# Kernel optimization log

Hardware: AMD Instinct MI355X
Metric: run time of the kernel (lower is better)

The kernel has to match this reference:

```python
import jax, jax.numpy as jnp
import numpy as np

P_DIMS = [100, 100, 80, 60, 60]
P = sum(P_DIMS)  # 400
N_STREAMS = len(P_DIMS)
MEM_ITERS = 5
DECAY = 0.8
LR = 0.5        # hebbian_learning_rate
FORGET = 0.9999 # hebbian_forget_rate
NEG_SLOPE = 0.01


def _build_masks():
    idx = np.cumsum([0] + P_DIMS)
    hier = np.zeros((P, P), np.float32)
    for i in range(N_STREAMS):
        for j in range(i, N_STREAMS):
            hier[idx[i]:idx[i + 1], idx[j]:idx[j + 1]] = 1.0
    iters = [MEM_ITERS - f for f in range(N_STREAMS)]  # [5,4,3,2,1]
    rmasks = np.zeros((MEM_ITERS, P), np.float32)
    for it in range(MEM_ITERS):
        for s, r in enumerate(iters):
            if it < r:
                rmasks[it, idx[s]:idx[s + 1]] = 1.0
    return jnp.asarray(hier), jnp.asarray(rmasks)


def setup_inputs() -> dict:
    key = jax.random.key(0)
    k1, k2, k3, k4 = jax.random.split(key, 4)
    B = 512
    return {
        'M_prev': jax.random.normal(k1, (B, P, P), dtype=jnp.float32) * 0.1,
        'p_inferred': jax.random.normal(k2, (B, P), dtype=jnp.float32),
        'p_generated': jax.random.normal(k3, (B, P), dtype=jnp.float32),
        'query': jax.random.normal(k4, (B, P), dtype=jnp.float32),
    }


def reference(M_prev, p_inferred, p_generated, query):
    hier_mask, retrieval_masks = _build_masks()

    # Hebbian update: M = clamp(forget*M_prev + lr*(p-phat)(p+phat)^T, -1, 1) * hier_mask
    outer = (p_inferred - p_generated)[:, :, None] * (p_inferred + p_generated)[:, None, :]
    M = jnp.clip(FORGET * M_prev + LR * outer, -1.0, 1.0) * hier_mask

    # Hierarchical attractor retrieval
    h = jax.nn.leaky_relu(jnp.clip(query, -1.0, 1.0), NEG_SLOPE)

    def step(h, mask):
        mv = jnp.einsum('bpq,bq->bp', M, h)
        upd = jax.nn.leaky_relu(jnp.clip(DECAY * h + mv, -1.0, 1.0), NEG_SLOPE)
        return (1.0 - mask) * h + mask * upd, None

    h, _ = jax.lax.scan(step, h, retrieval_masks)
    return h
```

## Files before the change

### kernel.cpp

```cpp
#include <hip/hip_runtime.h>


#define PDIM 400
#define CROWS 96
#define FORGET 0.9999f
#define LRATE  0.5f
#define DECAY  0.8f
#define SLOPE  0.01f

__device__ __forceinline__ float leaky_clip(float x) {
    x = fminf(fmaxf(x, -1.0f), 1.0f);
    return x > 0.0f ? x : SLOPE * x;
}
__device__ __forceinline__ float clamp1(float x) {
    return fminf(fmaxf(x, -1.0f), 1.0f);
}

__device__ __forceinline__ int c4beg(int p) {
    return (p < 100) ? 0 : (p < 200) ? 25 : (p < 280) ? 50 : (p < 340) ? 70 : 85;
}

__device__ __forceinline__ float wave_sum(float x) {
    x += __int_as_float(__builtin_amdgcn_update_dpp(0, __float_as_int(x), 0xB1,  0xf, 0xf, true));
    x += __int_as_float(__builtin_amdgcn_update_dpp(0, __float_as_int(x), 0x4E,  0xf, 0xf, true));
    x += __int_as_float(__builtin_amdgcn_update_dpp(0, __float_as_int(x), 0x141, 0xf, 0xf, true));
    x += __int_as_float(__builtin_amdgcn_update_dpp(0, __float_as_int(x), 0x140, 0xf, 0xf, true));
    x += __int_as_float(__builtin_amdgcn_update_dpp(0, __float_as_int(x), 0x142, 0xf, 0xf, true));
    x += __int_as_float(__builtin_amdgcn_update_dpp(0, __float_as_int(x), 0x143, 0xf, 0xf, true));
    return __int_as_float(__builtin_amdgcn_readlane(__float_as_int(x), 63));
}

__device__ __forceinline__ void load_row(const float* __restrict__ Mb,
                                         int p, int R, int l,
                                         int& c4, float4& A, float4& B) {
    const float4 z4 = make_float4(0.f, 0.f, 0.f, 0.f);
    c4 = 0; A = z4; B = z4;
    if (p < R) {
        c4 = c4beg(p);
        const float* __restrict__ row = Mb + (size_t)p * PDIM;
        if (l >= c4)                A = *(const float4*)(row + 4 * l);
        if (l < 36 && 64 + l >= c4) B = *(const float4*)(row + 256 + 4 * l);
    }
}

__global__ __launch_bounds__(512, 2)
void hier_mem_kernel(const float* __restrict__ M_prev,
                     const float* __restrict__ p_inf,
                     const float* __restrict__ p_gen,
                     const float* __restrict__ query,
                     float* __restrict__ out)
{
    __shared__ float s_mc[CROWS][PDIM];
    __shared__ float s_h[2][PDIM];
    __shared__ float s_la[PDIM];

    const int b   = blockIdx.x;
    const int tid = threadIdx.x;
    const int l   = tid & 63;
    const int wid = tid >> 6;
    const float* __restrict__ Mb = M_prev + (size_t)b * PDIM * PDIM;

    if (tid < PDIM) {
        const float pi = p_inf[b * PDIM + tid];
        const float pg = p_gen[b * PDIM + tid];
        s_la[tid]   = LRATE * (pi - pg);
        s_h[0][tid] = leaky_clip(query[b * PDIM + tid]);
    }

    const float4 z4 = make_float4(0.f, 0.f, 0.f, 0.f);
    const float4* __restrict__ pi4 = (const float4*)(p_inf + (size_t)b * PDIM);
    const float4* __restrict__ pg4 = (const float4*)(p_gen + (size_t)b * PDIM);
    float4 vA, vB = z4;
    {
        const float4 x = pi4[l], y = pg4[l];
        vA = make_float4(x.x + y.x, x.y + y.y, x.z + y.z, x.w + y.w);
        if (l < 36) {
            const float4 u = pi4[64 + l], v = pg4[64 + l];
            vB = make_float4(u.x + v.x, u.y + v.y, u.z + v.z, u.w + v.w);
        }
    }
    __syncthreads();

    {
        const float* __restrict__ hcur = s_h[0];
        float* __restrict__ hnew = s_h[1];
        float4 hA = *(const float4*)(hcur + 4 * l);
        float4 hB = z4;
        if (l < 36) hB = *(const float4*)(hcur + 256 + 4 * l);

        int p = wid;
        int c0, c1; float4 A0, B0, A1, B1;
        load_row(Mb, p,     PDIM, l, c0, A0, B0);
        load_row(Mb, p + 8, PDIM, l, c1, A1, B1);

        while (p < PDIM) {
            int c2; float4 A2, B2;
            load_row(Mb, p + 16, PDIM, l, c2, A2, B2);

            const float la = s_la[p];
            float acc = 0.f;
            float4 mA = z4, mB = z4;
            if (l >= c0) {
                mA.x = clamp1(fmaf(FORGET, A0.x, la * vA.x));
                mA.y = clamp1(fmaf(FORGET, A0.y, la * vA.y));
                mA.z = clamp1(fmaf(FORGET, A0.z, la * vA.z));
                mA.w = clamp1(fmaf(FORGET, A0.w, la * vA.w));
                acc = fmaf(mA.x, hA.x, fmaf(mA.y, hA.y, fmaf(mA.z, hA.z, mA.w * hA.w)));
            }
            if (l < 36 && 64 + l >= c0) {
                mB.x = clamp1(fmaf(FORGET, B0.x, la * vB.x));
                mB.y = clamp1(fmaf(FORGET, B0.y, la * vB.y));
                mB.z = clamp1(fmaf(FORGET, B0.z, la * vB.z));
                mB.w = clamp1(fmaf(FORGET, B0.w, la * vB.w));
                acc = fmaf(mB.x, hB.x, fmaf(mB.y, hB.y, fmaf(mB.z, hB.z, fmaf(mB.w, hB.w, acc))));
            }
            if (p < CROWS) {
                *(float4*)&s_mc[p][4 * l] = mA;
                if (l < 36) *(float4*)&s_mc[p][256 + 4 * l] = mB;
            }

            const float tot = wave_sum(acc);
            if (l == 0) {
                hnew[p] = leaky_clip(fmaf(DECAY, hcur[p], tot));
            }

            p += 8; c0 = c1; A0 = A1; B0 = B1; c1 = c2; A1 = A2; B1 = B2;
        }
        __syncthreads();
    }

    int cur = 1;
    const int Rt[4] = {340, 280, 200, 100};
    #pragma unroll
    for (int t = 0; t < 4; ++t) {
        const int R = Rt[t];
        const float* __restrict__ hcur = s_h[cur];
        float* __restrict__ hnew = s_h[cur ^ 1];

        float4 hA = *(const float4*)(hcur + 4 * l);
        float4 hB = z4;
        if (l < 36) hB = *(const float4*)(hcur + 256 + 4 * l);

        int sp = CROWS + wid;
        int c0, c1; float4 A0, B0, A1, B1;
        load_row(Mb, sp,     R, l, c0, A0, B0);
        load_row(Mb, sp + 8, R, l, c1, A1, B1);

        {
            int p = wid;
            float4 KA = *(const float4*)&s_mc[p][4 * l];
            float4 KB = z4;
            if (l < 36) KB = *(const float4*)&s_mc[p][256 + 4 * l];
            while (p < CROWS) {
                const int pn = p + 8;
                float4 NA = z4, NB = z4;
                if (pn < CROWS) {
                    NA = *(const float4*)&s_mc[pn][4 * l];
                    if (l < 36) NB = *(const float4*)&s_mc[pn][256 + 4 * l];
                }
                float acc = fmaf(KA.x, hA.x, fmaf(KA.y, hA.y, fmaf(KA.z, hA.z, KA.w * hA.w)));
                acc = fmaf(KB.x, hB.x, fmaf(KB.y, hB.y, fmaf(KB.z, hB.z, fmaf(KB.w, hB.w, acc))));
                const float tot = wave_sum(acc);
                if (l == 0) {
                    hnew[p] = leaky_clip(fmaf(DECAY, hcur[p], tot));
                }
                p = pn; KA = NA; KB = NB;
            }
        }

        while (sp < R) {
            int c2; float4 A2, B2;
            load_row(Mb, sp + 16, R, l, c2, A2, B2);

            const float la = s_la[sp];
            float acc = 0.f;
            if (l >= c0) {
                float m0 = clamp1(fmaf(FORGET, A0.x, la * vA.x));
                float m1 = clamp1(fmaf(FORGET, A0.y, la * vA.y));
                float m2 = clamp1(fmaf(FORGET, A0.z, la * vA.z));
                float m3 = clamp1(fmaf(FORGET, A0.w, la * vA.w));
                acc = fmaf(m0, hA.x, fmaf(m1, hA.y, fmaf(m2, hA.z, m3 * hA.w)));
            }
            if (l < 36 && 64 + l >= c0) {
                float m0 = clamp1(fmaf(FORGET, B0.x, la * vB.x));
                float m1 = clamp1(fmaf(FORGET, B0.y, la * vB.y));
                float m2 = clamp1(fmaf(FORGET, B0.z, la * vB.z));
                float m3 = clamp1(fmaf(FORGET, B0.w, la * vB.w));
                acc = fmaf(m0, hB.x, fmaf(m1, hB.y, fmaf(m2, hB.z, fmaf(m3, hB.w, acc))));
            }

            const float tot = wave_sum(acc);
            if (l == 0) {
                hnew[sp] = leaky_clip(fmaf(DECAY, hcur[sp], tot));
            }

            sp += 8; c0 = c1; A0 = A1; B0 = B1; c1 = c2; A1 = A2; B1 = B2;
        }

        if (tid >= R && tid < PDIM) hnew[tid] = hcur[tid];
        __syncthreads();
        cur ^= 1;
    }

    if (tid < PDIM) {
        out[b * PDIM + tid] = s_h[cur][tid];
    }
}

extern "C" void kernel_launch(void* const* d_in, const int* in_sizes, int n_in,
                              void* d_out, int out_size, void* d_ws, size_t ws_size,
                              hipStream_t stream) {
    const float* M_prev = (const float*)d_in[0];
    const float* p_inf  = (const float*)d_in[1];
    const float* p_gen  = (const float*)d_in[2];
    const float* query  = (const float*)d_in[3];
    float* out = (float*)d_out;

    const int B = in_sizes[1] / PDIM;
    hipLaunchKernelGGL(hier_mem_kernel, dim3(B), dim3(512), 0, stream,
                       M_prev, p_inf, p_gen, query, out);
}
```

Baseline: 503.7 us.

## Use packed FP32 math, shrink LDS row cache, raise occupancy to four blocks

Replaces scalar FMA chains with v_pk_fma/v_pk_mul packed FP32 inline asm. The shared-memory cache of updated M rows drops from 96 to 46 rows, and launch bounds now request 4 blocks per CU. Register prefetch depth in the later retrieval passes falls from two rows to one. The aim is more resident waves to hide global memory latency on the M_prev re-reads. In exchange, more rows must be re-read from global memory in each later pass, and prefetch depth per wave is lower.

```diff
diff --git a/kernel.cpp b/kernel.cpp
--- a/kernel.cpp
+++ b/kernel.cpp
@@ -2,18 +2,34 @@
 
 
 #define PDIM 400
-#define CROWS 96
+#define CROWS 46
 #define FORGET 0.9999f
 #define LRATE  0.5f
 #define DECAY  0.8f
 #define SLOPE  0.01f
 
+typedef float f32x2 __attribute__((ext_vector_type(2)));
+union V4 { float4 f4; f32x2 h2[2]; };
+
 __device__ __forceinline__ float leaky_clip(float x) {
     x = fminf(fmaxf(x, -1.0f), 1.0f);
     return x > 0.0f ? x : SLOPE * x;
 }
 __device__ __forceinline__ float clamp1(float x) {
     return fminf(fmaxf(x, -1.0f), 1.0f);
+}
+__device__ __forceinline__ f32x2 pk_mul(f32x2 a, f32x2 b) {
+    f32x2 d;
+    asm("v_pk_mul_f32 %0, %1, %2" : "=v"(d) : "v"(a), "v"(b));
+    return d;
+}
+__device__ __forceinline__ f32x2 pk_fma(f32x2 a, f32x2 b, f32x2 c) {
+    f32x2 d;
+    asm("v_pk_fma_f32 %0, %1, %2, %3" : "=v"(d) : "v"(a), "v"(b), "v"(c));
+    return d;
+}
+__device__ __forceinline__ f32x2 clamp2(f32x2 x) {
+    x.x = clamp1(x.x); x.y = clamp1(x.y); return x;
 }
 
 __device__ __forceinline__ int c4beg(int p) {
@@ -32,18 +48,19 @@
 
 __device__ __forceinline__ void load_row(const float* __restrict__ Mb,
                                          int p, int R, int l,
-                                         int& c4, float4& A, float4& B) {
-    const float4 z4 = make_float4(0.f, 0.f, 0.f, 0.f);
-    c4 = 0; A = z4; B = z4;
+                                         int& c4, V4& A, V4& B) {
+    A.f4 = make_float4(0.f, 0.f, 0.f, 0.f);
+    B.f4 = A.f4;
+    c4 = 0;
     if (p < R) {
         c4 = c4beg(p);
         const float* __restrict__ row = Mb + (size_t)p * PDIM;
-        if (l >= c4)                A = *(const float4*)(row + 4 * l);
-        if (l < 36 && 64 + l >= c4) B = *(const float4*)(row + 256 + 4 * l);
-    }
-}
-
-__global__ __launch_bounds__(512, 2)
+        if (l >= c4)                A.f4 = *(const float4*)(row + 4 * l);
+        if (l < 36 && 64 + l >= c4) B.f4 = *(const float4*)(row + 256 + 4 * l);
+    }
+}
+
+__global__ __launch_bounds__(512, 4)
 void hier_mem_kernel(const float* __restrict__ M_prev,
                      const float* __restrict__ p_inf,
                      const float* __restrict__ p_gen,
@@ -70,56 +87,56 @@
     const float4 z4 = make_float4(0.f, 0.f, 0.f, 0.f);
     const float4* __restrict__ pi4 = (const float4*)(p_inf + (size_t)b * PDIM);
     const float4* __restrict__ pg4 = (const float4*)(p_gen + (size_t)b * PDIM);
-    float4 vA, vB = z4;
+    V4 vA, vB; vB.f4 = z4;
     {
         const float4 x = pi4[l], y = pg4[l];
-        vA = make_float4(x.x + y.x, x.y + y.y, x.z + y.z, x.w + y.w);
+        vA.f4 = make_float4(x.x + y.x, x.y + y.y, x.z + y.z, x.w + y.w);
         if (l < 36) {
             const float4 u = pi4[64 + l], v = pg4[64 + l];
-            vB = make_float4(u.x + v.x, u.y + v.y, u.z + v.z, u.w + v.w);
-        }
-    }
+            vB.f4 = make_float4(u.x + v.x, u.y + v.y, u.z + v.z, u.w + v.w);
+        }
+    }
+    const f32x2 F2 = {FORGET, FORGET};
     __syncthreads();
 
     {
         const float* __restrict__ hcur = s_h[0];
         float* __restrict__ hnew = s_h[1];
-        float4 hA = *(const float4*)(hcur + 4 * l);
-        float4 hB = z4;
-        if (l < 36) hB = *(const float4*)(hcur + 256 + 4 * l);
+        V4 hA, hB; hB.f4 = z4;
+        hA.f4 = *(const float4*)(hcur + 4 * l);
+        if (l < 36) hB.f4 = *(const float4*)(hcur + 256 + 4 * l);
 
         int p = wid;
-        int c0, c1; float4 A0, B0, A1, B1;
+        int c0, c1; V4 A0, B0, A1, B1;
         load_row(Mb, p,     PDIM, l, c0, A0, B0);
         load_row(Mb, p + 8, PDIM, l, c1, A1, B1);
 
         while (p < PDIM) {
-            int c2; float4 A2, B2;
+            int c2; V4 A2, B2;
             load_row(Mb, p + 16, PDIM, l, c2, A2, B2);
 
             const float la = s_la[p];
-            float acc = 0.f;
-            float4 mA = z4, mB = z4;
+            const f32x2 la2 = {la, la};
+            f32x2 acc2 = {0.f, 0.f};
+            V4 mA, mB; mA.f4 = z4; mB.f4 = z4;
             if (l >= c0) {
-                mA.x = clamp1(fmaf(FORGET, A0.x, la * vA.x));
-                mA.y = clamp1(fmaf(FORGET, A0.y, la * vA.y));
-                mA.z = clamp1(fmaf(FORGET, A0.z, la * vA.z));
-                mA.w = clamp1(fmaf(FORGET, A0.w, la * vA.w));
-                acc = fmaf(mA.x, hA.x, fmaf(mA.y, hA.y, fmaf(mA.z, hA.z, mA.w * hA.w)));
+                mA.h2[0] = clamp2(pk_fma(F2, A0.h2[0], pk_mul(la2, vA.h2[0])));
+                mA.h2[1] = clamp2(pk_fma(F2, A0.h2[1], pk_mul(la2, vA.h2[1])));
+                acc2 = pk_fma(mA.h2[0], hA.h2[0], acc2);
+                acc2 = pk_fma(mA.h2[1], hA.h2[1], acc2);
             }
             if (l < 36 && 64 + l >= c0) {
-                mB.x = clamp1(fmaf(FORGET, B0.x, la * vB.x));
-                mB.y = clamp1(fmaf(FORGET, B0.y, la * vB.y));
-                mB.z = clamp1(fmaf(FORGET, B0.z, la * vB.z));
-                mB.w = clamp1(fmaf(FORGET, B0.w, la * vB.w));
-                acc = fmaf(mB.x, hB.x, fmaf(mB.y, hB.y, fmaf(mB.z, hB.z, fmaf(mB.w, hB.w, acc))));
+                mB.h2[0] = clamp2(pk_fma(F2, B0.h2[0], pk_mul(la2, vB.h2[0])));
+                mB.h2[1] = clamp2(pk_fma(F2, B0.h2[1], pk_mul(la2, vB.h2[1])));
+                acc2 = pk_fma(mB.h2[0], hB.h2[0], acc2);
+                acc2 = pk_fma(mB.h2[1], hB.h2[1], acc2);
             }
             if (p < CROWS) {
-                *(float4*)&s_mc[p][4 * l] = mA;
-                if (l < 36) *(float4*)&s_mc[p][256 + 4 * l] = mB;
-            }
-
-            const float tot = wave_sum(acc);
+                *(float4*)&s_mc[p][4 * l] = mA.f4;
+                if (l < 36) *(float4*)&s_mc[p][256 + 4 * l] = mB.f4;
+            }
+
+            const float tot = wave_sum(acc2.x + acc2.y);
             if (l == 0) {
                 hnew[p] = leaky_clip(fmaf(DECAY, hcur[p], tot));
             }
@@ -137,30 +154,31 @@
         const float* __restrict__ hcur = s_h[cur];
         float* __restrict__ hnew = s_h[cur ^ 1];
 
-        float4 hA = *(const float4*)(hcur + 4 * l);
-        float4 hB = z4;
-        if (l < 36) hB = *(const float4*)(hcur + 256 + 4 * l);
+        V4 hA, hB; hB.f4 = z4;
+        hA.f4 = *(const float4*)(hcur + 4 * l);
+        if (l < 36) hB.f4 = *(const float4*)(hcur + 256 + 4 * l);
 
         int sp = CROWS + wid;
-        int c0, c1; float4 A0, B0, A1, B1;
-        load_row(Mb, sp,     R, l, c0, A0, B0);
-        load_row(Mb, sp + 8, R, l, c1, A1, B1);
+        int c0; V4 A0, B0;
+        load_row(Mb, sp, R, l, c0, A0, B0);
 
         {
             int p = wid;
-            float4 KA = *(const float4*)&s_mc[p][4 * l];
-            float4 KB = z4;
-            if (l < 36) KB = *(const float4*)&s_mc[p][256 + 4 * l];
+            V4 KA, KB; KB.f4 = z4;
+            KA.f4 = *(const float4*)&s_mc[p][4 * l];
+            if (l < 36) KB.f4 = *(const float4*)&s_mc[p][256 + 4 * l];
             while (p < CROWS) {
                 const int pn = p + 8;
-                float4 NA = z4, NB = z4;
+                V4 NA, NB; NA.f4 = z4; NB.f4 = z4;
                 if (pn < CROWS) {
-                    NA = *(const float4*)&s_mc[pn][4 * l];
-                    if (l < 36) NB = *(const float4*)&s_mc[pn][256 + 4 * l];
+                    NA.f4 = *(const float4*)&s_mc[pn][4 * l];
+                    if (l < 36) NB.f4 = *(const float4*)&s_mc[pn][256 + 4 * l];
                 }
-                float acc = fmaf(KA.x, hA.x, fmaf(KA.y, hA.y, fmaf(KA.z, hA.z, KA.w * hA.w)));
-                acc = fmaf(KB.x, hB.x, fmaf(KB.y, hB.y, fmaf(KB.z, hB.z, fmaf(KB.w, hB.w, acc))));
-                const float tot = wave_sum(acc);
+                f32x2 acc2 = pk_fma(KA.h2[0], hA.h2[0],
+                             pk_fma(KA.h2[1], hA.h2[1],
+                             pk_fma(KB.h2[0], hB.h2[0],
+                             pk_mul(KB.h2[1], hB.h2[1]))));
+                const float tot = wave_sum(acc2.x + acc2.y);
                 if (l == 0) {
                     hnew[p] = leaky_clip(fmaf(DECAY, hcur[p], tot));
                 }
@@ -169,32 +187,31 @@
         }
 
         while (sp < R) {
-            int c2; float4 A2, B2;
-            load_row(Mb, sp + 16, R, l, c2, A2, B2);
+            int c1n; V4 A1, B1;
+            load_row(Mb, sp + 8, R, l, c1n, A1, B1);
 
             const float la = s_la[sp];
-            float acc = 0.f;
+            const f32x2 la2 = {la, la};
+            f32x2 acc2 = {0.f, 0.f};
             if (l >= c0) {
-                float m0 = clamp1(fmaf(FORGET, A0.x, la * vA.x));
-                float m1 = clamp1(fmaf(FORGET, A0.y, la * vA.y));
-                float m2 = clamp1(fmaf(FORGET, A0.z, la * vA.z));
-                float m3 = clamp1(fmaf(FORGET, A0.w, la * vA.w));
-                acc = fmaf(m0, hA.x, fmaf(m1, hA.y, fmaf(m2, hA.z, m3 * hA.w)));
+                f32x2 m0 = clamp2(pk_fma(F2, A0.h2[0], pk_mul(la2, vA.h2[0])));
+                f32x2 m1 = clamp2(pk_fma(F2, A0.h2[1], pk_mul(la2, vA.h2[1])));
+                acc2 = pk_fma(m0, hA.h2[0], acc2);
+                acc2 = pk_fma(m1, hA.h2[1], acc2);
             }
             if (l < 36 && 64 + l >= c0) {
-                float m0 = clamp1(fmaf(FORGET, B0.x, la * vB.x));
-                float m1 = clamp1(fmaf(FORGET, B0.y, la * vB.y));
-                float m2 = clamp1(fmaf(FORGET, B0.z, la * vB.z));
-                float m3 = clamp1(fmaf(FORGET, B0.w, la * vB.w));
-                acc = fmaf(m0, hB.x, fmaf(m1, hB.y, fmaf(m2, hB.z, fmaf(m3, hB.w, acc))));
-            }
-
-            const float tot = wave_sum(acc);
+                f32x2 m0 = clamp2(pk_fma(F2, B0.h2[0], pk_mul(la2, vB.h2[0])));
+                f32x2 m1 = clamp2(pk_fma(F2, B0.h2[1], pk_mul(la2, vB.h2[1])));
+                acc2 = pk_fma(m0, hB.h2[0], acc2);
+                acc2 = pk_fma(m1, hB.h2[1], acc2);
+            }
+
+            const float tot = wave_sum(acc2.x + acc2.y);
             if (l == 0) {
                 hnew[sp] = leaky_clip(fmaf(DECAY, hcur[sp], tot));
             }
 
-            sp += 8; c0 = c1; A0 = A1; B0 = B1; c1 = c2; A1 = A2; B1 = B2;
+            sp += 8; c0 = c1n; A0 = A1; B0 = B1;
         }
 
         if (tid >= R && tid < PDIM) hnew[tid] = hcur[tid];
```

Result: faster. 481.8 us (-4.3%).
